# Performance work log

Measured on AMD Instinct MI355X. Metric: run time of the kernel, lower is better.

## Reference

```python
import jax, jax.numpy as jnp
import numpy as np

TOKENS = 8192
HIDDEN = 6144
NUM_EXPERTS = 768  # n_routed_experts (512) + zero_expert_num (256)
TOP_K = 12
ROUTED_SCALING_FACTOR = 2.5


def setup_inputs() -> dict:
    key = jax.random.key(0)
    k1, k2, k3 = jax.random.split(key, 3)
    hidden_states = jax.random.normal(k1, (TOKENS, HIDDEN), dtype=jnp.float32)
    classifier_weight = jax.random.normal(k2, (NUM_EXPERTS, HIDDEN), dtype=jnp.float32) * (1.0 / np.sqrt(HIDDEN))
    e_score_correction_bias = jax.random.normal(k3, (NUM_EXPERTS,), dtype=jnp.float32) * 0.1
    return {
        "hidden_states": hidden_states,
        "classifier_weight": classifier_weight,
        "e_score_correction_bias": e_score_correction_bias,
    }


def reference(hidden_states, classifier_weight, e_score_correction_bias):
    # [T, H] -> router logits [T, E] in fp32 (source casts to float32)
    x = hidden_states.reshape(-1, HIDDEN).astype(jnp.float32)
    router_logits = jnp.einsum('th,eh->te', x, classifier_weight)

    # npu_moe_gating_top_k(renorm=0, norm_type=0): softmax scores,
    # bias-corrected selection, gather un-biased scores, scale.
    scores = jax.nn.softmax(router_logits, axis=-1)                # [T, E]
    scores_for_choice = scores + e_score_correction_bias[None, :]  # [T, E]
    _, topk_indices = jax.lax.top_k(scores_for_choice, TOP_K)       # [T, K]
    topk_weights = jnp.take_along_axis(scores, topk_indices, axis=-1)
    topk_weights = topk_weights * ROUTED_SCALING_FACTOR

    return topk_indices.astype(jnp.int32), topk_weights
```

## Files before the change

### kernel.cpp

```cpp
#include <hip/hip_runtime.h>

#define TOKENS  8192
#define HIDDEN  6144
#define EXPERTS 768
#define TOPK    12
#define RSF     2.5f
#define ROWH    (HIDDEN * 2)

typedef float    f4 __attribute__((ext_vector_type(4)));
typedef _Float16 h8 __attribute__((ext_vector_type(8)));
typedef _Float16 h2 __attribute__((ext_vector_type(2)));
typedef __fp16   g2 __attribute__((ext_vector_type(2)));

#define BM 128
#define BN 96
#define BK 32
#define NKT (HIDDEN / BK)
#define BUFH 14336
#define LOH  7168
#define LO_SCALE 4096.0f
#define LO_INV   2.44140625e-4f

static __device__ inline h2 pk(float a, float b) {
    g2 r = __builtin_amdgcn_cvt_pkrtz(a, b);
    return __builtin_bit_cast(h2, r);
}

static __device__ inline void cvt8(const f4 a, const f4 b, h8& hi, h8& lo) {
    h2 ha = pk(a.x, a.y), hb = pk(a.z, a.w), hc = pk(b.x, b.y), hd = pk(b.z, b.w);
    h2 la = pk((a.x - (float)ha[0]) * LO_SCALE, (a.y - (float)ha[1]) * LO_SCALE);
    h2 lb = pk((a.z - (float)hb[0]) * LO_SCALE, (a.w - (float)hb[1]) * LO_SCALE);
    h2 lc = pk((b.x - (float)hc[0]) * LO_SCALE, (b.y - (float)hc[1]) * LO_SCALE);
    h2 ld = pk((b.z - (float)hd[0]) * LO_SCALE, (b.w - (float)hd[1]) * LO_SCALE);
    hi[0]=ha[0]; hi[1]=ha[1]; hi[2]=hb[0]; hi[3]=hb[1];
    hi[4]=hc[0]; hi[5]=hc[1]; hi[6]=hd[0]; hi[7]=hd[1];
    lo[0]=la[0]; lo[1]=la[1]; lo[2]=lb[0]; lo[3]=lb[1];
    lo[4]=lc[0]; lo[5]=lc[1]; lo[6]=ld[0]; lo[7]=ld[1];
}

__global__ __launch_bounds__(256)
void split_convert(const float* X, const float* W, _Float16* XO, _Float16* WO) {
    const size_t GX = (size_t)TOKENS * HIDDEN / 8;
    const size_t GW = (size_t)EXPERTS * HIDDEN / 8;
    size_t gid = (size_t)blockIdx.x * 256 + threadIdx.x;
    if (gid >= GX + GW) return;
    const float* src; _Float16* dst;
    if (gid < GX) { src = X + gid * 8;        dst = XO + gid * 16; }
    else          { size_t l = gid - GX; src = W + l * 8; dst = WO + l * 16; }
    const f4* p = (const f4*)src;
    f4 a = p[0], b = p[1];
    h8 hi, lo;
    cvt8(a, b, hi, lo);
    h8* o = (h8*)dst;
    o[0] = hi; o[1] = lo;
}

typedef __attribute__((address_space(1))) const void av1;
typedef __attribute__((address_space(3))) void av3;
static __device__ inline void stage16(const void* g, void* l) {
    __builtin_amdgcn_global_load_lds((av1*)g, (av3*)l, 16, 0, 0);
}

__global__ __launch_bounds__(256, 2)
void router_gemm(const _Float16* __restrict__ Xs, const _Float16* __restrict__ Ws,
                 float* __restrict__ L) {
    __shared__ _Float16 sm[2 * BUFH];

    const int t    = threadIdx.x;
    const int bm   = blockIdx.x * BM;
    const int bn   = blockIdx.y * BN;
    const int lane = t & 63;
    const int w    = t >> 6;
    const int lr   = lane & 15;
    const int lq   = lane >> 4;

    const _Float16* ps[7];
    uint32_t        ldso[7];
#pragma unroll
    for (int q = 0; q < 7; ++q) {
        const int j    = w * 7 + q;
        const int isLo = (j >= 14);
        const int jj   = isLo ? j - 14 : j;
        const int r    = jj * 16 + (lane >> 2);
        const int p    = lane & 3;
        const int g    = p ^ ((r >> 1) & 3);
        const _Float16* row = (r < BM) ? (Xs + (size_t)(bm + r) * ROWH)
                                       : (Ws + (size_t)(bn + r - BM) * ROWH);
        ps[q]   = row + g * 16 + isLo * 8;
        ldso[q] = (uint32_t)(isLo * LOH + jj * 512);
    }

    uint32_t aoff[4], boff[3];
#pragma unroll
    for (int mi = 0; mi < 4; ++mi) {
        const int r = (w & 1) * 64 + mi * 16 + lr;
        aoff[mi] = r * 32 + ((lq ^ ((r >> 1) & 3)) * 8);
    }
#pragma unroll
    for (int ni = 0; ni < 3; ++ni) {
        const int r = 128 + (w >> 1) * 48 + ni * 16 + lr;
        boff[ni] = r * 32 + ((lq ^ ((r >> 1) & 3)) * 8);
    }

    f4 acc_h[4][3], acc_c[4][3];
#pragma unroll
    for (int i = 0; i < 4; ++i)
#pragma unroll
        for (int j = 0; j < 3; ++j) { acc_h[i][j] = f4{0,0,0,0}; acc_c[i][j] = f4{0,0,0,0}; }

#pragma unroll
    for (int q = 0; q < 7; ++q) {
        stage16((const void*)ps[q], (void*)(sm + ldso[q]));
        ps[q] += 64;
    }

    auto do_tile = [&](const uint32_t boR, const uint32_t boW, const bool doStage) {
        if (doStage) {
#pragma unroll
            for (int q = 0; q < 7; ++q) {
                stage16((const void*)ps[q], (void*)(sm + boW + ldso[q]));
                ps[q] += 64;
            }
            asm volatile("s_waitcnt vmcnt(7)" ::: "memory");
        } else {
            asm volatile("s_waitcnt vmcnt(0)" ::: "memory");
        }
        asm volatile("s_barrier" ::: "memory");

        h8 ah[4], al[4], bh[3], bl[3];
#pragma unroll
        for (int mi = 0; mi < 4; ++mi) {
            ah[mi] = *(const h8*)(sm + boR + aoff[mi]);
            al[mi] = *(const h8*)(sm + boR + aoff[mi] + LOH);
        }
#pragma unroll
        for (int ni = 0; ni < 3; ++ni) {
            bh[ni] = *(const h8*)(sm + boR + boff[ni]);
            bl[ni] = *(const h8*)(sm + boR + boff[ni] + LOH);
        }
        __builtin_amdgcn_s_setprio(1);
#pragma unroll
        for (int mi = 0; mi < 4; ++mi)
#pragma unroll
            for (int ni = 0; ni < 3; ++ni) {
                acc_h[mi][ni] = __builtin_amdgcn_mfma_f32_16x16x32_f16(ah[mi], bh[ni], acc_h[mi][ni], 0, 0, 0);
                acc_c[mi][ni] = __builtin_amdgcn_mfma_f32_16x16x32_f16(ah[mi], bl[ni], acc_c[mi][ni], 0, 0, 0);
                acc_c[mi][ni] = __builtin_amdgcn_mfma_f32_16x16x32_f16(al[mi], bh[ni], acc_c[mi][ni], 0, 0, 0);
            }
        __builtin_amdgcn_s_setprio(0);
        asm volatile("s_barrier" ::: "memory");
    };

    for (int T2 = 0; T2 < NKT / 2; ++T2) {
        do_tile(0u, (uint32_t)BUFH, true);
        do_tile((uint32_t)BUFH, 0u, T2 != NKT / 2 - 1);
    }

#pragma unroll
    for (int mi = 0; mi < 4; ++mi)
#pragma unroll
        for (int ni = 0; ni < 3; ++ni)
#pragma unroll
            for (int r = 0; r < 4; ++r) {
                const int gm = bm + (w & 1) * 64 + mi * 16 + lq * 4 + r;
                const int gn = bn + (w >> 1) * 48 + ni * 16 + lr;
                L[(size_t)gm * EXPERTS + gn] = acc_h[mi][ni][r] + acc_c[mi][ni][r] * LO_INV;
            }
}

__global__ __launch_bounds__(256)
void router_topk(const float* __restrict__ L, const float* __restrict__ bias,
                 float* __restrict__ outIdx, float* __restrict__ outW) {
    __shared__ float sb[EXPERTS];
    const int t = threadIdx.x;
    for (int i = t; i < EXPERTS; i += 256) sb[i] = bias[i];
    __syncthreads();

    const int lane  = t & 63;
    const int wave  = t >> 6;
    const int token = blockIdx.x * 4 + wave;
    const float* row = L + (size_t)token * EXPERTS;

    float lg[12];
#pragma unroll
    for (int j = 0; j < 12; ++j) lg[j] = row[lane + 64 * j];

    float m = lg[0];
#pragma unroll
    for (int j = 1; j < 12; ++j) m = fmaxf(m, lg[j]);
#pragma unroll
    for (int o = 32; o > 0; o >>= 1) m = fmaxf(m, __shfl_xor(m, o));

    float s = 0.0f;
#pragma unroll
    for (int j = 0; j < 12; ++j) { lg[j] = __expf(lg[j] - m); s += lg[j]; }
#pragma unroll
    for (int o = 32; o > 0; o >>= 1) s += __shfl_xor(s, o);
    const float inv = 1.0f / s;

    float cand[12];
#pragma unroll
    for (int j = 0; j < 12; ++j) {
        lg[j] *= inv;
        cand[j] = lg[j] + sb[lane + 64 * j];
    }

#pragma unroll
    for (int r = 0; r < TOPK; ++r) {
        float bv = -__builtin_inff();
        int   bi = EXPERTS;
#pragma unroll
        for (int j = 0; j < 12; ++j) {
            const int e = lane + 64 * j;
            const bool better = (cand[j] > bv) || (cand[j] == bv && e < bi);
            bv = better ? cand[j] : bv;
            bi = better ? e : bi;
        }
#pragma unroll
        for (int o = 32; o > 0; o >>= 1) {
            const float ov = __shfl_xor(bv, o);
            const int   oi = __shfl_xor(bi, o);
            const bool better = (ov > bv) || (ov == bv && oi < bi);
            bv = better ? ov : bv;
            bi = better ? oi : bi;
        }
        if (lane == 0) {
            outIdx[token * TOPK + r] = (float)bi;
            outW  [token * TOPK + r] = (bv - sb[bi]) * RSF;
        }
        if ((bi & 63) == lane) {
            const int slot = bi >> 6;
#pragma unroll
            for (int j = 0; j < 12; ++j)
                if (j == slot) cand[j] = -__builtin_inff();
        }
    }
}

extern "C" void kernel_launch(void* const* d_in, const int* in_sizes, int n_in,
                              void* d_out, int out_size, void* d_ws, size_t ws_size,
                              hipStream_t stream) {
    float* X = (float*)d_in[0];
    float* W = (float*)d_in[1];
    const float* B = (const float*)d_in[2];

    const size_t bytesX = (size_t)TOKENS * HIDDEN * sizeof(float);
    const size_t bytesW = (size_t)EXPERTS * HIDDEN * sizeof(float);
    const size_t bytesL = (size_t)TOKENS * EXPERTS * sizeof(float);

    _Float16* Xs; _Float16* Ws; float* logits;
    if (ws_size >= bytesX + bytesW + bytesL) {
        char* p = (char*)d_ws;
        Xs     = (_Float16*)p;
        Ws     = (_Float16*)(p + bytesX);
        logits = (float*)(p + bytesX + bytesW);
    } else {
        Xs     = (_Float16*)X;
        Ws     = (_Float16*)W;
        logits = (float*)d_ws;
    }

    float* outIdx = (float*)d_out;
    float* outW   = outIdx + (size_t)TOKENS * TOPK;

    const int ngroups = (TOKENS + EXPERTS) * HIDDEN / 8;
    split_convert<<<ngroups / 256, 256, 0, stream>>>(X, W, Xs, Ws);

    dim3 grid_gemm(TOKENS / BM, EXPERTS / BN);
    router_gemm<<<grid_gemm, 256, 0, stream>>>((const _Float16*)Xs, (const _Float16*)Ws, logits);
    router_topk<<<TOKENS / 4, 256, 0, stream>>>(logits, B, outIdx, outW);
}
```

Baseline: 567.3 us.

## Load A operand directly to registers and split hi/lo per row

Result: slower. 806.7 us (+42.2%).

```diff
diff --git a/kernel.cpp b/kernel.cpp
--- a/kernel.cpp
+++ b/kernel.cpp
@@ -14,10 +14,9 @@
 
 #define BM 128
 #define BN 96
-#define BK 32
-#define NKT (HIDDEN / BK)
-#define BUFH 14336
-#define LOH  7168
+#define NKT 192
+#define BUFB 6144
+#define BLO  3072
 #define LO_SCALE 4096.0f
 #define LO_INV   2.44140625e-4f
 
@@ -40,19 +39,26 @@
 
 __global__ __launch_bounds__(256)
 void split_convert(const float* X, const float* W, _Float16* XO, _Float16* WO) {
-    const size_t GX = (size_t)TOKENS * HIDDEN / 8;
-    const size_t GW = (size_t)EXPERTS * HIDDEN / 8;
-    size_t gid = (size_t)blockIdx.x * 256 + threadIdx.x;
-    if (gid >= GX + GW) return;
+    const int row = blockIdx.x;
     const float* src; _Float16* dst;
-    if (gid < GX) { src = X + gid * 8;        dst = XO + gid * 16; }
-    else          { size_t l = gid - GX; src = W + l * 8; dst = WO + l * 16; }
-    const f4* p = (const f4*)src;
-    f4 a = p[0], b = p[1];
-    h8 hi, lo;
-    cvt8(a, b, hi, lo);
-    h8* o = (h8*)dst;
-    o[0] = hi; o[1] = lo;
+    if (row < TOKENS) { src = X + (size_t)row * HIDDEN;            dst = XO + (size_t)row * ROWH; }
+    else              { src = W + (size_t)(row - TOKENS) * HIDDEN; dst = WO + (size_t)(row - TOKENS) * ROWH; }
+    const int t = threadIdx.x;
+    f4 a[3], b[3];
+#pragma unroll
+    for (int i = 0; i < 3; ++i) {
+        const f4* p = (const f4*)(src + (size_t)(t + 256 * i) * 8);
+        a[i] = p[0]; b[i] = p[1];
+    }
+    __syncthreads();
+#pragma unroll
+    for (int i = 0; i < 3; ++i) {
+        h8 hi, lo;
+        cvt8(a[i], b[i], hi, lo);
+        const int g = t + 256 * i;
+        *(h8*)(dst + (size_t)g * 8)          = hi;
+        *(h8*)(dst + HIDDEN + (size_t)g * 8) = lo;
+    }
 }
 
 typedef __attribute__((address_space(1))) const void av1;
@@ -64,7 +70,7 @@
 __global__ __launch_bounds__(256, 2)
 void router_gemm(const _Float16* __restrict__ Xs, const _Float16* __restrict__ Ws,
                  float* __restrict__ L) {
-    __shared__ _Float16 sm[2 * BUFH];
+    __shared__ _Float16 sm[2 * BUFB];
 
     const int t    = threadIdx.x;
     const int bm   = blockIdx.x * BM;
@@ -74,86 +80,90 @@
     const int lr   = lane & 15;
     const int lq   = lane >> 4;
 
-    const _Float16* ps[7];
-    uint32_t        ldso[7];
-#pragma unroll
-    for (int q = 0; q < 7; ++q) {
-        const int j    = w * 7 + q;
-        const int isLo = (j >= 14);
-        const int jj   = isLo ? j - 14 : j;
+    const _Float16* ps[3];
+    uint32_t        ldso[3];
+#pragma unroll
+    for (int q = 0; q < 3; ++q) {
+        const int j    = w * 3 + q;
+        const int isLo = (j >= 6);
+        const int jj   = isLo ? j - 6 : j;
         const int r    = jj * 16 + (lane >> 2);
         const int p    = lane & 3;
         const int g    = p ^ ((r >> 1) & 3);
-        const _Float16* row = (r < BM) ? (Xs + (size_t)(bm + r) * ROWH)
-                                       : (Ws + (size_t)(bn + r - BM) * ROWH);
-        ps[q]   = row + g * 16 + isLo * 8;
-        ldso[q] = (uint32_t)(isLo * LOH + jj * 512);
-    }
-
-    uint32_t aoff[4], boff[3];
+        ps[q]   = Ws + (size_t)(bn + r) * ROWH + g * 8 + isLo * HIDDEN;
+        ldso[q] = (uint32_t)(isLo * BLO + jj * 512);
+    }
+
+    const _Float16* pa[4];
+#pragma unroll
+    for (int mi = 0; mi < 4; ++mi)
+        pa[mi] = Xs + (size_t)(bm + (w & 1) * 64 + mi * 16 + lr) * ROWH + lq * 8;
+
+    uint32_t boff[3];
+#pragma unroll
+    for (int ni = 0; ni < 3; ++ni) {
+        const int r = (w >> 1) * 48 + ni * 16 + lr;
+        boff[ni] = r * 32 + ((lq ^ ((r >> 1) & 3)) * 8);
+    }
+
+    f4 acc_h[4][3], acc_c[4][3];
+#pragma unroll
+    for (int i = 0; i < 4; ++i)
+#pragma unroll
+        for (int j = 0; j < 3; ++j) { acc_h[i][j] = f4{0,0,0,0}; acc_c[i][j] = f4{0,0,0,0}; }
+
+    h8 Ah0[4], Al0[4], Ah1[4], Al1[4];
+
+#pragma unroll
+    for (int q = 0; q < 3; ++q) { stage16((const void*)ps[q], (void*)(sm + ldso[q])); ps[q] += 32; }
+    __builtin_amdgcn_sched_barrier(0);
 #pragma unroll
     for (int mi = 0; mi < 4; ++mi) {
-        const int r = (w & 1) * 64 + mi * 16 + lr;
-        aoff[mi] = r * 32 + ((lq ^ ((r >> 1) & 3)) * 8);
-    }
-#pragma unroll
-    for (int ni = 0; ni < 3; ++ni) {
-        const int r = 128 + (w >> 1) * 48 + ni * 16 + lr;
-        boff[ni] = r * 32 + ((lq ^ ((r >> 1) & 3)) * 8);
-    }
-
-    f4 acc_h[4][3], acc_c[4][3];
-#pragma unroll
-    for (int i = 0; i < 4; ++i)
-#pragma unroll
-        for (int j = 0; j < 3; ++j) { acc_h[i][j] = f4{0,0,0,0}; acc_c[i][j] = f4{0,0,0,0}; }
-
-#pragma unroll
-    for (int q = 0; q < 7; ++q) {
-        stage16((const void*)ps[q], (void*)(sm + ldso[q]));
-        ps[q] += 64;
-    }
-
-    auto do_tile = [&](const uint32_t boR, const uint32_t boW, const bool doStage) {
-        if (doStage) {
-#pragma unroll
-            for (int q = 0; q < 7; ++q) {
-                stage16((const void*)ps[q], (void*)(sm + boW + ldso[q]));
-                ps[q] += 64;
+        Ah0[mi] = *(const h8*)(pa[mi]);
+        Al0[mi] = *(const h8*)(pa[mi] + HIDDEN);
+    }
+    asm volatile("s_waitcnt vmcnt(8)" ::: "memory");
+    __builtin_amdgcn_sched_barrier(0);
+    asm volatile("s_barrier" ::: "memory");
+
+    auto tile = [&](const uint32_t bR, const uint32_t bW, const uint32_t koN,
+                    h8 (&AhC)[4], h8 (&AlC)[4], h8 (&AhN)[4], h8 (&AlN)[4],
+                    const bool doNext) {
+        if (doNext) {
+#pragma unroll
+            for (int q = 0; q < 3; ++q) { stage16((const void*)ps[q], (void*)(sm + bW + ldso[q])); ps[q] += 32; }
+            __builtin_amdgcn_sched_barrier(0);
+#pragma unroll
+            for (int mi = 0; mi < 4; ++mi) {
+                AhN[mi] = *(const h8*)(pa[mi] + koN);
+                AlN[mi] = *(const h8*)(pa[mi] + koN + HIDDEN);
             }
-            asm volatile("s_waitcnt vmcnt(7)" ::: "memory");
-        } else {
-            asm volatile("s_waitcnt vmcnt(0)" ::: "memory");
-        }
-        asm volatile("s_barrier" ::: "memory");
-
-        h8 ah[4], al[4], bh[3], bl[3];
-#pragma unroll
-        for (int mi = 0; mi < 4; ++mi) {
-            ah[mi] = *(const h8*)(sm + boR + aoff[mi]);
-            al[mi] = *(const h8*)(sm + boR + aoff[mi] + LOH);
-        }
+        }
+        h8 bh[3], bl[3];
 #pragma unroll
         for (int ni = 0; ni < 3; ++ni) {
-            bh[ni] = *(const h8*)(sm + boR + boff[ni]);
-            bl[ni] = *(const h8*)(sm + boR + boff[ni] + LOH);
-        }
-        __builtin_amdgcn_s_setprio(1);
+            bh[ni] = *(const h8*)(sm + bR + boff[ni]);
+            bl[ni] = *(const h8*)(sm + bR + boff[ni] + BLO);
+        }
 #pragma unroll
         for (int mi = 0; mi < 4; ++mi)
 #pragma unroll
             for (int ni = 0; ni < 3; ++ni) {
-                acc_h[mi][ni] = __builtin_amdgcn_mfma_f32_16x16x32_f16(ah[mi], bh[ni], acc_h[mi][ni], 0, 0, 0);
-                acc_c[mi][ni] = __builtin_amdgcn_mfma_f32_16x16x32_f16(ah[mi], bl[ni], acc_c[mi][ni], 0, 0, 0);
-                acc_c[mi][ni] = __builtin_amdgcn_mfma_f32_16x16x32_f16(al[mi], bh[ni], acc_c[mi][ni], 0, 0, 0);
+                acc_h[mi][ni] = __builtin_amdgcn_mfma_f32_16x16x32_f16(AhC[mi], bh[ni], acc_h[mi][ni], 0, 0, 0);
+                acc_c[mi][ni] = __builtin_amdgcn_mfma_f32_16x16x32_f16(AhC[mi], bl[ni], acc_c[mi][ni], 0, 0, 0);
+                acc_c[mi][ni] = __builtin_amdgcn_mfma_f32_16x16x32_f16(AlC[mi], bh[ni], acc_c[mi][ni], 0, 0, 0);
             }
-        __builtin_amdgcn_s_setprio(0);
-        asm volatile("s_barrier" ::: "memory");
+        if (doNext) {
+            asm volatile("s_waitcnt vmcnt(8) lgkmcnt(0)" ::: "memory");
+            __builtin_amdgcn_sched_barrier(0);
+            asm volatile("s_barrier" ::: "memory");
+        }
     };
 
+    uint32_t ko = 32;
     for (int T2 = 0; T2 < NKT / 2; ++T2) {
-        do_tile(0u, (uint32_t)BUFH, true);
-        do_tile((uint32_t)BUFH, 0u, T2 != NKT / 2 - 1);
+        tile(0u, (uint32_t)BUFB, ko, Ah0, Al0, Ah1, Al1, true);              ko += 32;
+        tile((uint32_t)BUFB, 0u, ko, Ah1, Al1, Ah0, Al0, T2 != NKT / 2 - 1); ko += 32;
     }
 
 #pragma unroll
@@ -263,8 +273,7 @@
     float* outIdx = (float*)d_out;
     float* outW   = outIdx + (size_t)TOKENS * TOPK;
 
-    const int ngroups = (TOKENS + EXPERTS) * HIDDEN / 8;
-    split_convert<<<ngroups / 256, 256, 0, stream>>>(X, W, Xs, Ws);
+    split_convert<<<TOKENS + EXPERTS, 256, 0, stream>>>(X, W, Xs, Ws);
 
     dim3 grid_gemm(TOKENS / BM, EXPERTS / BN);
     router_gemm<<<grid_gemm, 256, 0, stream>>>((const _Float16*)Xs, (const _Float16*)Ws, logits);
```
